# Optimization experiments

Hardware: AMD Instinct MI355X
Metric: run time of the kernel (lower is better)

The kernel has to match this reference:

```python
import jax, jax.numpy as jnp
import numpy as np


def _make_coord(n):
    # grid-center coords in (-1, 1), matching make_coord in the torch code
    return -1.0 + 1.0 / n + (2.0 / n) * jnp.arange(n, dtype=jnp.float32)


def _mlp(inp, W1, b1, W2, b2, W3, b3):
    h = jax.nn.relu(inp @ W1 + b1)
    h = jax.nn.relu(h @ W2 + b2)
    return h @ W3 + b3


def setup_inputs() -> dict:
    key = jax.random.key(0)
    ks = jax.random.split(key, 4)
    dim = 64
    x = jax.random.normal(ks[0], (4, dim, 64, 64), dtype=jnp.float32)
    W1 = jax.random.normal(ks[1], (dim + 2, 256), dtype=jnp.float32) * 0.05
    W2 = jax.random.normal(ks[2], (256, 256), dtype=jnp.float32) * 0.05
    W3 = jax.random.normal(ks[3], (256, dim), dtype=jnp.float32) * 0.05
    return {
        "x": x,
        "W1": W1, "b1": jnp.zeros((256,), jnp.float32),
        "W2": W2, "b2": jnp.zeros((256,), jnp.float32),
        "W3": W3, "b3": jnp.zeros((dim,), jnp.float32),
        "h_out": 256, "w_out": 256,
    }


def reference(x, W1, b1, W2, b2, W3, b3, h_out, w_out):
    B, C, H, W = x.shape
    # query coords on the output grid (same for every batch element)
    gy, gx = jnp.meshgrid(_make_coord(h_out), _make_coord(w_out), indexing="ij")
    cy = gy.reshape(-1)  # [Q], coord channel 0 (height)
    cx = gx.reshape(-1)  # [Q], coord channel 1 (width)
    rx = 1.0 / H  # = 2 / H / 2
    ry = 1.0 / W
    eps_shift = 1e-6
    lim = 1.0 - 1e-6
    fy = _make_coord(H)  # feat_coord values along height
    fx = _make_coord(W)

    preds = []
    areas = []
    for vx in (-1.0, 1.0):
        for vy in (-1.0, 1.0):
            sy = jnp.clip(cy + vx * rx + eps_shift, -lim, lim)
            sx = jnp.clip(cx + vy * ry + eps_shift, -lim, lim)
            # grid_sample nearest, align_corners=False: unnormalize then round
            iy = jnp.clip(jnp.round(((sy + 1.0) * H - 1.0) * 0.5), 0, H - 1).astype(jnp.int32)
            ix = jnp.clip(jnp.round(((sx + 1.0) * W - 1.0) * 0.5), 0, W - 1).astype(jnp.int32)
            q_feat = x[:, :, iy, ix].transpose(0, 2, 1)  # [B, Q, C]
            rel_y = (cy - fy[iy]) * H  # [Q]
            rel_x = (cx - fx[ix]) * W
            rel = jnp.stack([rel_y, rel_x], axis=-1)  # [Q, 2]
            inp = jnp.concatenate(
                [q_feat, jnp.broadcast_to(rel, (B,) + rel.shape)], axis=-1
            )  # [B, Q, C+2]
            preds.append(_mlp(inp, W1, b1, W2, b2, W3, b3))  # [B, Q, C]
            areas.append(jnp.abs(rel_y * rel_x) + 1e-9)  # [Q]

    tot_area = areas[0] + areas[1] + areas[2] + areas[3]
    # local_ensemble swap: 0<->3, 1<->2 (opposite-corner area weighting)
    areas = [areas[3], areas[2], areas[1], areas[0]]
    ret = 0.0
    for pred, area in zip(preds, areas):
        ret = ret + pred * (area / tot_area)[None, :, None]
    return ret  # [B, h_out*w_out, C]
```

## Files before the change

kernel.cpp:

```cpp
#include <hip/hip_runtime.h>


typedef __bf16 bf16x8 __attribute__((ext_vector_type(8)));
typedef float  f32x4  __attribute__((ext_vector_type(4)));
typedef unsigned int u32x2 __attribute__((ext_vector_type(2)));

#define LDS_SWZ(row, kbyte) ((kbyte) ^ (((row) & 7) << 4))

#define WP1_U 0
#define WP2_U (48 * 512)
#define WP3_U (176 * 512)
#define XT_OFF (1 << 20)

__global__ __launch_bounds__(64) void prep_weights(
    const float* __restrict__ W1, const float* __restrict__ W2,
    const float* __restrict__ W3, ushort* __restrict__ ws)
{
    const int blk = blockIdx.x;
    const int l   = threadIdx.x;
    const float* W; int Kreal, N, ks, nt; size_t off;
    if (blk < 48)       { W = W1; Kreal = 66;  N = 256; ks = blk >> 4;  nt = blk & 15; off = WP1_U + (size_t)blk * 512; }
    else if (blk < 176) { int b2 = blk - 48;  W = W2; Kreal = 256; N = 256; ks = b2 >> 4; nt = b2 & 15; off = WP2_U + (size_t)b2 * 512; }
    else                { int b3 = blk - 176; W = W3; Kreal = 256; N = 64;  ks = b3 >> 2; nt = b3 & 3;  off = WP3_U + (size_t)b3 * 512; }

    const int n = nt * 16 + (l & 15);
    ushort v[8];
    #pragma unroll
    for (int j = 0; j < 8; ++j) {
        const int k = ks * 32 + ((l >> 4) * 8) + j;
        const float f = (k < Kreal) ? W[(size_t)k * N + n] : 0.0f;
        v[j] = __builtin_bit_cast(ushort, (__bf16)f);
    }
    *(uint4*)(ws + off + (size_t)l * 8) = *(const uint4*)v;
}

__global__ __launch_bounds__(256) void prep_xt(const float* __restrict__ x, char* __restrict__ xt)
{
    const int blk = blockIdx.x;
    const int b = blk >> 6, iy = blk & 63;
    const int ix = threadIdx.x & 63, cq = threadIdx.x >> 6;
    ushort v[16];
    #pragma unroll
    for (int j = 0; j < 16; ++j) {
        const int ch = cq * 16 + j;
        const float f = x[(((size_t)b * 64 + ch) * 64 + iy) * 64 + ix];
        v[j] = __builtin_bit_cast(ushort, (__bf16)f);
    }
    char* dst = xt + ((size_t)((b * 4096 + iy * 64 + ix)) * 128) + cq * 32;
    *(uint4*)dst        = *(const uint4*)(v);
    *(uint4*)(dst + 16) = *(const uint4*)(v + 8);
}

__device__ inline unsigned pk2(float a, float b) {
    return (unsigned)__builtin_bit_cast(ushort, (__bf16)a)
         | ((unsigned)__builtin_bit_cast(ushort, (__bf16)b) << 16);
}

__global__ __launch_bounds__(512, 2) void liif_mfma12_kernel(
    const char* __restrict__ xt,
    const float* __restrict__ b1f, const float* __restrict__ b2f, const float* __restrict__ b3f,
    const ushort* __restrict__ ws, float* __restrict__ out)
{
    __shared__ char bufH[64 * 1024];

    const int tid  = threadIdx.x;
    const int lane = tid & 63;
    const int wv   = tid >> 6;
    const int lrow = lane & 15;
    const int lk   = lane >> 4;
    const int mh   = wv >> 2;
    const int nq   = wv & 3;
    const int wtile4 = nq * 4;

    const int bid0 = blockIdx.x;
    const int b    = (bid0 & 7) >> 1;
    const int qidx = (bid0 >> 3) * 2 + (bid0 & 1);
    const int q0   = qidx << 5;

    int   pixT[4];
    float relyT[4], relxT[4], wgtT[4];
    #pragma unroll
    for (int s = 0; s < 2; ++s) {
        const int q  = q0 + s * 16 + lrow;
        const int yq = q >> 8, xq = q & 255;
        const float cy  = -1.0f + (2.0f * yq + 1.0f) / 256.0f;
        const float cx  = -1.0f + (2.0f * xq + 1.0f) / 256.0f;
        const float lim = 1.0f - 1e-6f;
        float area[4];
        #pragma unroll
        for (int c = 0; c < 4; ++c) {
            const float vx = (c & 2) ? 1.0f : -1.0f;
            const float vy = (c & 1) ? 1.0f : -1.0f;
            float sy = cy + vx * (1.0f / 64.0f) + 1e-6f;
            float sx = cx + vy * (1.0f / 64.0f) + 1e-6f;
            sy = fminf(fmaxf(sy, -lim), lim);
            sx = fminf(fmaxf(sx, -lim), lim);
            int iyv = (int)rintf(((sy + 1.0f) * 64.0f - 1.0f) * 0.5f);
            int ixv = (int)rintf(((sx + 1.0f) * 64.0f - 1.0f) * 0.5f);
            iyv = min(max(iyv, 0), 63);
            ixv = min(max(ixv, 0), 63);
            const float fy = -1.0f + (2.0f * iyv + 1.0f) / 64.0f;
            const float fx = -1.0f + (2.0f * ixv + 1.0f) / 64.0f;
            const float ry = (cy - fy) * 64.0f;
            const float rx = (cx - fx) * 64.0f;
            area[c] = fabsf(ry * rx) + 1e-9f;
            if ((c >> 1) == mh) {
                const int nt = ((c & 1) << 1) | s;
                pixT[nt]  = (b * 4096 + iyv * 64 + ixv) * 128;
                relyT[nt] = ry;
                relxT[nt] = rx;
            }
        }
        const float tot = area[0] + area[1] + area[2] + area[3];
        #pragma unroll
        for (int c = 0; c < 4; ++c) {
            if ((c >> 1) == mh) {
                const int nt = ((c & 1) << 1) | s;
                wgtT[nt] = area[3 - c] / tot;
            }
        }
    }

    f32x4 acc[4][4];

    {
        #pragma unroll
        for (int mt = 0; mt < 4; ++mt) {
            const f32x4 bs = *(const f32x4*)(b1f + (wtile4 + mt) * 16 + lk * 4);
            #pragma unroll
            for (int nt = 0; nt < 4; ++nt) acc[mt][nt] = bs;
        }
        const ushort* wpl = ws + WP1_U + ((size_t)wtile4 << 9) + (lane << 3);
        #pragma unroll 1
        for (int ks = 0; ks < 2; ++ks) {
            bf16x8 wa[4];
            #pragma unroll
            for (int mt = 0; mt < 4; ++mt)
                wa[mt] = *(const bf16x8*)(wpl + ((size_t)(ks * 16 + mt) << 9));
            #pragma unroll
            for (int nt = 0; nt < 4; ++nt) {
                const bf16x8 hb = *(const bf16x8*)(xt + pixT[nt] + ks * 64 + lk * 16);
                __builtin_amdgcn_s_setprio(1);
                #pragma unroll
                for (int mt = 0; mt < 4; ++mt)
                    acc[mt][nt] = __builtin_amdgcn_mfma_f32_16x16x32_bf16(wa[mt], hb, acc[mt][nt], 0, 0, 0);
                __builtin_amdgcn_s_setprio(0);
            }
        }
        {
            bf16x8 wa[4];
            #pragma unroll
            for (int mt = 0; mt < 4; ++mt)
                wa[mt] = *(const bf16x8*)(wpl + ((size_t)(32 + mt) << 9));
            #pragma unroll
            for (int nt = 0; nt < 4; ++nt) {
                bf16x8 hb = (bf16x8){0, 0, 0, 0, 0, 0, 0, 0};
                if (lk == 0) { hb[0] = (__bf16)relyT[nt]; hb[1] = (__bf16)relxT[nt]; }
                __builtin_amdgcn_s_setprio(1);
                #pragma unroll
                for (int mt = 0; mt < 4; ++mt)
                    acc[mt][nt] = __builtin_amdgcn_mfma_f32_16x16x32_bf16(wa[mt], hb, acc[mt][nt], 0, 0, 0);
                __builtin_amdgcn_s_setprio(0);
            }
        }
    }
    {
        #pragma unroll
        for (int nt = 0; nt < 4; ++nt) {
            const int row = mh * 64 + nt * 16 + lrow;
            #pragma unroll
            for (int mt = 0; mt < 4; ++mt) {
                const int nb = ((wtile4 + mt) * 16 + lk * 4) * 2;
                u32x2 p;
                p[0] = pk2(fmaxf(acc[mt][nt][0], 0.0f), fmaxf(acc[mt][nt][1], 0.0f));
                p[1] = pk2(fmaxf(acc[mt][nt][2], 0.0f), fmaxf(acc[mt][nt][3], 0.0f));
                *(u32x2*)(bufH + row * 512 + LDS_SWZ(row, nb)) = p;
            }
        }
    }
    __syncthreads();

    {
        #pragma unroll
        for (int mt = 0; mt < 4; ++mt) {
            const f32x4 bs = *(const f32x4*)(b2f + (wtile4 + mt) * 16 + lk * 4);
            #pragma unroll
            for (int nt = 0; nt < 4; ++nt) acc[mt][nt] = bs;
        }
        const ushort* wpl = ws + WP2_U + ((size_t)wtile4 << 9) + (lane << 3);
        #pragma unroll 1
        for (int ks = 0; ks < 8; ++ks) {
            bf16x8 wa[4];
            #pragma unroll
            for (int mt = 0; mt < 4; ++mt)
                wa[mt] = *(const bf16x8*)(wpl + ((size_t)(ks * 16 + mt) << 9));
            #pragma unroll
            for (int nt = 0; nt < 4; ++nt) {
                const int row   = mh * 64 + nt * 16 + lrow;
                const int kbyte = ks * 64 + lk * 16;
                const bf16x8 hb = *(const bf16x8*)(bufH + row * 512 + LDS_SWZ(row, kbyte));
                __builtin_amdgcn_s_setprio(1);
                #pragma unroll
                for (int mt = 0; mt < 4; ++mt)
                    acc[mt][nt] = __builtin_amdgcn_mfma_f32_16x16x32_bf16(wa[mt], hb, acc[mt][nt], 0, 0, 0);
                __builtin_amdgcn_s_setprio(0);
            }
        }
    }
    __syncthreads();
    {
        #pragma unroll
        for (int nt = 0; nt < 4; ++nt) {
            const int row = mh * 64 + nt * 16 + lrow;
            #pragma unroll
            for (int mt = 0; mt < 4; ++mt) {
                const int nb = ((wtile4 + mt) * 16 + lk * 4) * 2;
                u32x2 p;
                p[0] = pk2(fmaxf(acc[mt][nt][0], 0.0f), fmaxf(acc[mt][nt][1], 0.0f));
                p[1] = pk2(fmaxf(acc[mt][nt][2], 0.0f), fmaxf(acc[mt][nt][3], 0.0f));
                *(u32x2*)(bufH + row * 512 + LDS_SWZ(row, nb)) = p;
            }
        }
    }
    __syncthreads();

    {
        f32x4 acc3[4];
        const f32x4 bs3 = *(const f32x4*)(b3f + nq * 16 + lk * 4);
        #pragma unroll
        for (int mt = 0; mt < 4; ++mt) acc3[mt] = bs3;

        const ushort* wp3 = ws + WP3_U + (lane << 3);
        #pragma unroll 1
        for (int ks = 0; ks < 8; ++ks) {
            const bf16x8 wa = *(const bf16x8*)(wp3 + ((size_t)(ks * 4 + nq) << 9));
            #pragma unroll
            for (int mt = 0; mt < 4; ++mt) {
                const int row   = mh * 64 + mt * 16 + lrow;
                const int kbyte = ks * 64 + lk * 16;
                const bf16x8 hb = *(const bf16x8*)(bufH + row * 512 + LDS_SWZ(row, kbyte));
                __builtin_amdgcn_s_setprio(1);
                acc3[mt] = __builtin_amdgcn_mfma_f32_16x16x32_bf16(wa, hb, acc3[mt], 0, 0, 0);
                __builtin_amdgcn_s_setprio(0);
            }
        }
        __syncthreads();
        #pragma unroll
        for (int mt = 0; mt < 4; ++mt) {
            const int row = mh * 64 + mt * 16 + lrow;
            const f32x4 v = acc3[mt] * wgtT[mt];
            const int cb = nq * 64 + lk * 16;
            *(f32x4*)(bufH + row * 256 + LDS_SWZ(row, cb)) = v;
        }
    }
    __syncthreads();

    {
        const int q  = tid >> 4;
        const int ch = (tid & 15) * 4;
        f32x4 sum = (f32x4){0.f, 0.f, 0.f, 0.f};
        #pragma unroll
        for (int c = 0; c < 4; ++c) {
            const int row = c * 32 + q;
            const f32x4 v = *(const f32x4*)(bufH + row * 256 + LDS_SWZ(row, ch * 4));
            sum += v;
        }
        *(f32x4*)(out + ((size_t)b * 65536 + q0 + q) * 64 + ch) = sum;
    }
}

extern "C" void kernel_launch(void* const* d_in, const int* in_sizes, int n_in,
                              void* d_out, int out_size, void* d_ws, size_t ws_size,
                              hipStream_t stream) {
    const float* x  = (const float*)d_in[0];
    const float* W1 = (const float*)d_in[1];
    const float* b1 = (const float*)d_in[2];
    const float* W2 = (const float*)d_in[3];
    const float* b2 = (const float*)d_in[4];
    const float* W3 = (const float*)d_in[5];
    const float* b3 = (const float*)d_in[6];
    float* out = (float*)d_out;
    ushort* wp = (ushort*)d_ws;
    char* xt   = (char*)d_ws + XT_OFF;

    prep_weights<<<208, 64, 0, stream>>>(W1, W2, W3, wp);
    prep_xt<<<256, 256, 0, stream>>>(x, xt);
    liif_mfma12_kernel<<<8192, 512, 0, stream>>>(xt, b1, b2, b3, wp, out);
}
```

Measured before the change: 241.1 us.

## Switch MLP to 32x32x16 MFMA with smaller blocks and fold coord inputs into FP32 bias

Restructures the fused MLP kernel to use 32x32x16 bf16 MFMA tiles instead of 16x16x32. Blocks shrink to 256 threads covering 16 queries (64 rows), with 32KB LDS and a launch bound allowing 3 blocks per SM. The two relative-coordinate inputs of layer 1 are now applied in FP32 as a bias-like initialisation instead of a padded extra K-step MFMA, which drops a third of layer-1 K work. The risks are different register pressure from the 16-wide accumulators and weights being reloaded by twice as many blocks.

```diff
diff --git a/kernel.cpp b/kernel.cpp
--- a/kernel.cpp
+++ b/kernel.cpp
@@ -3,13 +3,14 @@
 
 typedef __bf16 bf16x8 __attribute__((ext_vector_type(8)));
 typedef float  f32x4  __attribute__((ext_vector_type(4)));
+typedef float  f32x16 __attribute__((ext_vector_type(16)));
 typedef unsigned int u32x2 __attribute__((ext_vector_type(2)));
 
 #define LDS_SWZ(row, kbyte) ((kbyte) ^ (((row) & 7) << 4))
 
 #define WP1_U 0
-#define WP2_U (48 * 512)
-#define WP3_U (176 * 512)
+#define WP2_U (32 * 512)
+#define WP3_U (160 * 512)
 #define XT_OFF (1 << 20)
 
 __global__ __launch_bounds__(64) void prep_weights(
@@ -18,18 +19,17 @@
 {
     const int blk = blockIdx.x;
     const int l   = threadIdx.x;
-    const float* W; int Kreal, N, ks, nt; size_t off;
-    if (blk < 48)       { W = W1; Kreal = 66;  N = 256; ks = blk >> 4;  nt = blk & 15; off = WP1_U + (size_t)blk * 512; }
-    else if (blk < 176) { int b2 = blk - 48;  W = W2; Kreal = 256; N = 256; ks = b2 >> 4; nt = b2 & 15; off = WP2_U + (size_t)b2 * 512; }
-    else                { int b3 = blk - 176; W = W3; Kreal = 256; N = 64;  ks = b3 >> 2; nt = b3 & 3;  off = WP3_U + (size_t)b3 * 512; }
-
-    const int n = nt * 16 + (l & 15);
+    const float* W; int N, ks, nt; size_t off;
+    if (blk < 32)       { W = W1; N = 256; ks = blk >> 3;  nt = blk & 7; off = WP1_U + (size_t)blk * 512; }
+    else if (blk < 160) { int b2 = blk - 32;  W = W2; N = 256; ks = b2 >> 3; nt = b2 & 7; off = WP2_U + (size_t)b2 * 512; }
+    else                { int b3 = blk - 160; W = W3; N = 64;  ks = b3 >> 1; nt = b3 & 1; off = WP3_U + (size_t)b3 * 512; }
+
+    const int n = nt * 32 + (l & 31);
     ushort v[8];
     #pragma unroll
     for (int j = 0; j < 8; ++j) {
-        const int k = ks * 32 + ((l >> 4) * 8) + j;
-        const float f = (k < Kreal) ? W[(size_t)k * N + n] : 0.0f;
-        v[j] = __builtin_bit_cast(ushort, (__bf16)f);
+        const int k = ks * 16 + ((l >> 5) * 8) + j;
+        v[j] = __builtin_bit_cast(ushort, (__bf16)W[(size_t)k * N + n]);
     }
     *(uint4*)(ws + off + (size_t)l * 8) = *(const uint4*)v;
 }
@@ -56,32 +56,30 @@
          | ((unsigned)__builtin_bit_cast(ushort, (__bf16)b) << 16);
 }
 
-__global__ __launch_bounds__(512, 2) void liif_mfma12_kernel(
-    const char* __restrict__ xt,
+__global__ __launch_bounds__(256, 3) void liif_mfma13_kernel(
+    const char* __restrict__ xt, const float* __restrict__ W1raw,
     const float* __restrict__ b1f, const float* __restrict__ b2f, const float* __restrict__ b3f,
     const ushort* __restrict__ ws, float* __restrict__ out)
 {
-    __shared__ char bufH[64 * 1024];
+    __shared__ char bufH[32 * 1024];
 
     const int tid  = threadIdx.x;
     const int lane = tid & 63;
     const int wv   = tid >> 6;
-    const int lrow = lane & 15;
-    const int lk   = lane >> 4;
-    const int mh   = wv >> 2;
-    const int nq   = wv & 3;
-    const int wtile4 = nq * 4;
+    const int l31  = lane & 31;
+    const int lhi  = lane >> 5;
+    const int cbit = (lane >> 4) & 1;
+    const int wbase = wv * 64;
 
     const int bid0 = blockIdx.x;
     const int b    = (bid0 & 7) >> 1;
     const int qidx = (bid0 >> 3) * 2 + (bid0 & 1);
-    const int q0   = qidx << 5;
-
-    int   pixT[4];
-    float relyT[4], relxT[4], wgtT[4];
-    #pragma unroll
-    for (int s = 0; s < 2; ++s) {
-        const int q  = q0 + s * 16 + lrow;
+    const int q0   = qidx << 4;
+
+    int   pixT[2];
+    float relyT[2], relxT[2], wgtT[2];
+    {
+        const int q  = q0 + (lane & 15);
         const int yq = q >> 8, xq = q & 255;
         const float cy  = -1.0f + (2.0f * yq + 1.0f) / 256.0f;
         const float cx  = -1.0f + (2.0f * xq + 1.0f) / 256.0f;
@@ -104,77 +102,74 @@
             const float ry = (cy - fy) * 64.0f;
             const float rx = (cx - fx) * 64.0f;
             area[c] = fabsf(ry * rx) + 1e-9f;
-            if ((c >> 1) == mh) {
-                const int nt = ((c & 1) << 1) | s;
-                pixT[nt]  = (b * 4096 + iyv * 64 + ixv) * 128;
-                relyT[nt] = ry;
-                relxT[nt] = rx;
+            if ((c & 1) == cbit) {
+                const int mt = c >> 1;
+                pixT[mt]  = (b * 4096 + iyv * 64 + ixv) * 128;
+                relyT[mt] = ry;
+                relxT[mt] = rx;
             }
         }
         const float tot = area[0] + area[1] + area[2] + area[3];
         #pragma unroll
-        for (int c = 0; c < 4; ++c) {
-            if ((c >> 1) == mh) {
-                const int nt = ((c & 1) << 1) | s;
-                wgtT[nt] = area[3 - c] / tot;
-            }
-        }
-    }
-
-    f32x4 acc[4][4];
-
-    {
-        #pragma unroll
-        for (int mt = 0; mt < 4; ++mt) {
-            const f32x4 bs = *(const f32x4*)(b1f + (wtile4 + mt) * 16 + lk * 4);
-            #pragma unroll
-            for (int nt = 0; nt < 4; ++nt) acc[mt][nt] = bs;
-        }
-        const ushort* wpl = ws + WP1_U + ((size_t)wtile4 << 9) + (lane << 3);
+        for (int c = 0; c < 4; ++c)
+            if ((c & 1) == cbit) wgtT[c >> 1] = area[3 - c] / tot;
+    }
+
+    f32x16 acc[2][2];
+
+    {
+        const float* w1y = W1raw + 64 * 256;
+        const float* w1x = W1raw + 65 * 256;
+        #pragma unroll
+        for (int nt = 0; nt < 2; ++nt) {
+            #pragma unroll
+            for (int g = 0; g < 4; ++g) {
+                const int nb = wbase + nt * 32 + 8 * g + 4 * lhi;
+                const f32x4 bs = *(const f32x4*)(b1f + nb);
+                const f32x4 wy = *(const f32x4*)(w1y + nb);
+                const f32x4 wx = *(const f32x4*)(w1x + nb);
+                #pragma unroll
+                for (int mt = 0; mt < 2; ++mt) {
+                    const f32x4 v = bs + relyT[mt] * wy + relxT[mt] * wx;
+                    acc[mt][nt][4 * g + 0] = v[0];
+                    acc[mt][nt][4 * g + 1] = v[1];
+                    acc[mt][nt][4 * g + 2] = v[2];
+                    acc[mt][nt][4 * g + 3] = v[3];
+                }
+            }
+        }
+        const ushort* wpl = ws + WP1_U + (lane << 3);
         #pragma unroll 1
-        for (int ks = 0; ks < 2; ++ks) {
-            bf16x8 wa[4];
-            #pragma unroll
-            for (int mt = 0; mt < 4; ++mt)
-                wa[mt] = *(const bf16x8*)(wpl + ((size_t)(ks * 16 + mt) << 9));
-            #pragma unroll
-            for (int nt = 0; nt < 4; ++nt) {
-                const bf16x8 hb = *(const bf16x8*)(xt + pixT[nt] + ks * 64 + lk * 16);
+        for (int ks = 0; ks < 4; ++ks) {
+            bf16x8 wa[2];
+            #pragma unroll
+            for (int nt = 0; nt < 2; ++nt)
+                wa[nt] = *(const bf16x8*)(wpl + ((size_t)(ks * 8 + wv * 2 + nt) << 9));
+            #pragma unroll
+            for (int mt = 0; mt < 2; ++mt) {
+                const bf16x8 hb = *(const bf16x8*)(xt + pixT[mt] + ks * 32 + lhi * 16);
                 __builtin_amdgcn_s_setprio(1);
                 #pragma unroll
-                for (int mt = 0; mt < 4; ++mt)
-                    acc[mt][nt] = __builtin_amdgcn_mfma_f32_16x16x32_bf16(wa[mt], hb, acc[mt][nt], 0, 0, 0);
+                for (int nt = 0; nt < 2; ++nt)
+                    acc[mt][nt] = __builtin_amdgcn_mfma_f32_32x32x16_bf16(wa[nt], hb, acc[mt][nt], 0, 0, 0);
                 __builtin_amdgcn_s_setprio(0);
             }
         }
-        {
-            bf16x8 wa[4];
-            #pragma unroll
-            for (int mt = 0; mt < 4; ++mt)
-                wa[mt] = *(const bf16x8*)(wpl + ((size_t)(32 + mt) << 9));
-            #pragma unroll
-            for (int nt = 0; nt < 4; ++nt) {
-                bf16x8 hb = (bf16x8){0, 0, 0, 0, 0, 0, 0, 0};
-                if (lk == 0) { hb[0] = (__bf16)relyT[nt]; hb[1] = (__bf16)relxT[nt]; }
-                __builtin_amdgcn_s_setprio(1);
-                #pragma unroll
-                for (int mt = 0; mt < 4; ++mt)
-                    acc[mt][nt] = __builtin_amdgcn_mfma_f32_16x16x32_bf16(wa[mt], hb, acc[mt][nt], 0, 0, 0);
-                __builtin_amdgcn_s_setprio(0);
-            }
-        }
-    }
-    {
-        #pragma unroll
-        for (int nt = 0; nt < 4; ++nt) {
-            const int row = mh * 64 + nt * 16 + lrow;
-            #pragma unroll
-            for (int mt = 0; mt < 4; ++mt) {
-                const int nb = ((wtile4 + mt) * 16 + lk * 4) * 2;
-                u32x2 p;
-                p[0] = pk2(fmaxf(acc[mt][nt][0], 0.0f), fmaxf(acc[mt][nt][1], 0.0f));
-                p[1] = pk2(fmaxf(acc[mt][nt][2], 0.0f), fmaxf(acc[mt][nt][3], 0.0f));
-                *(u32x2*)(bufH + row * 512 + LDS_SWZ(row, nb)) = p;
+    }
+    {
+        #pragma unroll
+        for (int mt = 0; mt < 2; ++mt) {
+            const int row = mt * 32 + l31;
+            #pragma unroll
+            for (int nt = 0; nt < 2; ++nt) {
+                #pragma unroll
+                for (int g = 0; g < 4; ++g) {
+                    const int nb = (wbase + nt * 32 + 8 * g + 4 * lhi) * 2;
+                    u32x2 p;
+                    p[0] = pk2(fmaxf(acc[mt][nt][4 * g + 0], 0.0f), fmaxf(acc[mt][nt][4 * g + 1], 0.0f));
+                    p[1] = pk2(fmaxf(acc[mt][nt][4 * g + 2], 0.0f), fmaxf(acc[mt][nt][4 * g + 3], 0.0f));
+                    *(u32x2*)(bufH + row * 512 + LDS_SWZ(row, nb)) = p;
+                }
             }
         }
     }
@@ -182,27 +177,35 @@
 
     {
         #pragma unroll
-        for (int mt = 0; mt < 4; ++mt) {
-            const f32x4 bs = *(const f32x4*)(b2f + (wtile4 + mt) * 16 + lk * 4);
-            #pragma unroll
-            for (int nt = 0; nt < 4; ++nt) acc[mt][nt] = bs;
-        }
-        const ushort* wpl = ws + WP2_U + ((size_t)wtile4 << 9) + (lane << 3);
+        for (int nt = 0; nt < 2; ++nt) {
+            #pragma unroll
+            for (int g = 0; g < 4; ++g) {
+                const f32x4 bs = *(const f32x4*)(b2f + wbase + nt * 32 + 8 * g + 4 * lhi);
+                #pragma unroll
+                for (int mt = 0; mt < 2; ++mt) {
+                    acc[mt][nt][4 * g + 0] = bs[0];
+                    acc[mt][nt][4 * g + 1] = bs[1];
+                    acc[mt][nt][4 * g + 2] = bs[2];
+                    acc[mt][nt][4 * g + 3] = bs[3];
+                }
+            }
+        }
+        const ushort* wpl = ws + WP2_U + (lane << 3);
         #pragma unroll 1
-        for (int ks = 0; ks < 8; ++ks) {
-            bf16x8 wa[4];
-            #pragma unroll
-            for (int mt = 0; mt < 4; ++mt)
-                wa[mt] = *(const bf16x8*)(wpl + ((size_t)(ks * 16 + mt) << 9));
-            #pragma unroll
-            for (int nt = 0; nt < 4; ++nt) {
-                const int row   = mh * 64 + nt * 16 + lrow;
-                const int kbyte = ks * 64 + lk * 16;
+        for (int ks = 0; ks < 16; ++ks) {
+            bf16x8 wa[2];
+            #pragma unroll
+            for (int nt = 0; nt < 2; ++nt)
+                wa[nt] = *(const bf16x8*)(wpl + ((size_t)(ks * 8 + wv * 2 + nt) << 9));
+            #pragma unroll
+            for (int mt = 0; mt < 2; ++mt) {
+                const int row = mt * 32 + l31;
+                const int kbyte = ks * 32 + lhi * 16;
                 const bf16x8 hb = *(const bf16x8*)(bufH + row * 512 + LDS_SWZ(row, kbyte));
                 __builtin_amdgcn_s_setprio(1);
                 #pragma unroll
-                for (int mt = 0; mt < 4; ++mt)
-                    acc[mt][nt] = __builtin_amdgcn_mfma_f32_16x16x32_bf16(wa[mt], hb, acc[mt][nt], 0, 0, 0);
+                for (int nt = 0; nt < 2; ++nt)
+                    acc[mt][nt] = __builtin_amdgcn_mfma_f32_32x32x16_bf16(wa[nt], hb, acc[mt][nt], 0, 0, 0);
                 __builtin_amdgcn_s_setprio(0);
             }
         }
@@ -210,46 +213,56 @@
     __syncthreads();
     {
         #pragma unroll
-        for (int nt = 0; nt < 4; ++nt) {
-            const int row = mh * 64 + nt * 16 + lrow;
-            #pragma unroll
-            for (int mt = 0; mt < 4; ++mt) {
-                const int nb = ((wtile4 + mt) * 16 + lk * 4) * 2;
-                u32x2 p;
-                p[0] = pk2(fmaxf(acc[mt][nt][0], 0.0f), fmaxf(acc[mt][nt][1], 0.0f));
-                p[1] = pk2(fmaxf(acc[mt][nt][2], 0.0f), fmaxf(acc[mt][nt][3], 0.0f));
-                *(u32x2*)(bufH + row * 512 + LDS_SWZ(row, nb)) = p;
+        for (int mt = 0; mt < 2; ++mt) {
+            const int row = mt * 32 + l31;
+            #pragma unroll
+            for (int nt = 0; nt < 2; ++nt) {
+                #pragma unroll
+                for (int g = 0; g < 4; ++g) {
+                    const int nb = (wbase + nt * 32 + 8 * g + 4 * lhi) * 2;
+                    u32x2 p;
+                    p[0] = pk2(fmaxf(acc[mt][nt][4 * g + 0], 0.0f), fmaxf(acc[mt][nt][4 * g + 1], 0.0f));
+                    p[1] = pk2(fmaxf(acc[mt][nt][4 * g + 2], 0.0f), fmaxf(acc[mt][nt][4 * g + 3], 0.0f));
+                    *(u32x2*)(bufH + row * 512 + LDS_SWZ(row, nb)) = p;
+                }
             }
         }
     }
     __syncthreads();
 
     {
-        f32x4 acc3[4];
-        const f32x4 bs3 = *(const f32x4*)(b3f + nq * 16 + lk * 4);
-        #pragma unroll
-        for (int mt = 0; mt < 4; ++mt) acc3[mt] = bs3;
-
+        const int mt3 = wv >> 1;
+        const int nt3 = wv & 1;
+        const int row = mt3 * 32 + l31;
+        f32x16 acc3;
+        #pragma unroll
+        for (int g = 0; g < 4; ++g) {
+            const f32x4 bs = *(const f32x4*)(b3f + nt3 * 32 + 8 * g + 4 * lhi);
+            acc3[4 * g + 0] = bs[0];
+            acc3[4 * g + 1] = bs[1];
+            acc3[4 * g + 2] = bs[2];
+            acc3[4 * g + 3] = bs[3];
+        }
         const ushort* wp3 = ws + WP3_U + (lane << 3);
         #pragma unroll 1
-        for (int ks = 0; ks < 8; ++ks) {
-            const bf16x8 wa = *(const bf16x8*)(wp3 + ((size_t)(ks * 4 + nq) << 9));
-            #pragma unroll
-            for (int mt = 0; mt < 4; ++mt) {
-                const int row   = mh * 64 + mt * 16 + lrow;
-                const int kbyte = ks * 64 + lk * 16;
-                const bf16x8 hb = *(const bf16x8*)(bufH + row * 512 + LDS_SWZ(row, kbyte));
-                __builtin_amdgcn_s_setprio(1);
-                acc3[mt] = __builtin_amdgcn_mfma_f32_16x16x32_bf16(wa, hb, acc3[mt], 0, 0, 0);
-                __builtin_amdgcn_s_setprio(0);
-            }
+        for (int ks = 0; ks < 16; ++ks) {
+            const bf16x8 wa = *(const bf16x8*)(wp3 + ((size_t)(ks * 2 + nt3) << 9));
+            const int kbyte = ks * 32 + lhi * 16;
+            const bf16x8 hb = *(const bf16x8*)(bufH + row * 512 + LDS_SWZ(row, kbyte));
+            __builtin_amdgcn_s_setprio(1);
+            acc3 = __builtin_amdgcn_mfma_f32_32x32x16_bf16(wa, hb, acc3, 0, 0, 0);
+            __builtin_amdgcn_s_setprio(0);
         }
         __syncthreads();
-        #pragma unroll
-        for (int mt = 0; mt < 4; ++mt) {
-            const int row = mh * 64 + mt * 16 + lrow;
-            const f32x4 v = acc3[mt] * wgtT[mt];
-            const int cb = nq * 64 + lk * 16;
+        const float wgt = wgtT[mt3];
+        #pragma unroll
+        for (int g = 0; g < 4; ++g) {
+            const int cb = (nt3 * 32 + 8 * g + 4 * lhi) * 4;
+            f32x4 v;
+            v[0] = acc3[4 * g + 0] * wgt;
+            v[1] = acc3[4 * g + 1] * wgt;
+            v[2] = acc3[4 * g + 2] * wgt;
+            v[3] = acc3[4 * g + 3] * wgt;
             *(f32x4*)(bufH + row * 256 + LDS_SWZ(row, cb)) = v;
         }
     }
@@ -261,7 +274,7 @@
         f32x4 sum = (f32x4){0.f, 0.f, 0.f, 0.f};
         #pragma unroll
         for (int c = 0; c < 4; ++c) {
-            const int row = c * 32 + q;
+            const int row = c * 16 + q;
             const f32x4 v = *(const f32x4*)(bufH + row * 256 + LDS_SWZ(row, ch * 4));
             sum += v;
         }
@@ -283,7 +296,7 @@
     ushort* wp = (ushort*)d_ws;
     char* xt   = (char*)d_ws + XT_OFF;
 
-    prep_weights<<<208, 64, 0, stream>>>(W1, W2, W3, wp);
+    prep_weights<<<192, 64, 0, stream>>>(W1, W2, W3, wp);
     prep_xt<<<256, 256, 0, stream>>>(x, xt);
-    liif_mfma12_kernel<<<8192, 512, 0, stream>>>(xt, b1, b2, b3, wp, out);
-}
+    liif_mfma13_kernel<<<16384, 256, 0, stream>>>(xt, W1, b1, b2, b3, wp, out);
+}
```

Result: slower. 299.2 us (+24.1%).
